# Kernel optimization log

Measured on AMD Instinct MI355X. Metric: run time of the kernel, lower is better.

The kernel has to match this reference:

```python
import jax, jax.numpy as jnp
import numpy as np

HEADS = 16
DIM_HEAD = 64
MAX_FREQ = 256.0  # lucidrains RotaryEmbedding(freqs_for='pixel', max_freq=256)


def axial_freqs(H, W, dim_head):
    # per-axis rotary dim = dim_head // 2 (RotaryEmbedding(dim=head_dim//2))
    d = dim_head // 2
    base = jnp.linspace(1.0, MAX_FREQ / 2.0, d // 2) * jnp.pi  # (d/2,)

    def axis(n):
        pos = jnp.linspace(-1.0, 1.0, n)              # pixel positions
        f = pos[:, None] * base                        # (n, d/2)
        return jnp.repeat(f, 2, axis=-1)               # (n, d) interleaved pairs

    fh = jnp.broadcast_to(axis(H)[:, None, :], (H, W, d))
    fw = jnp.broadcast_to(axis(W)[None, :, :], (H, W, d))
    return jnp.concatenate([fh, fw], axis=-1)          # (H, W, dim_head)


def apply_rope(t, freqs):
    # t: (B,T,H,W,h,d); freqs: (H,W,d)
    f = freqs[:, :, None, :]                           # broadcast over heads
    x = t.reshape(t.shape[:-1] + (t.shape[-1] // 2, 2))
    x1, x2 = x[..., 0], x[..., 1]
    rot = jnp.stack([-x2, x1], axis=-1).reshape(t.shape)  # rotate_half (interleaved)
    return t * jnp.cos(f) + rot * jnp.sin(f)


def setup_inputs() -> dict:
    key = jax.random.key(0)
    k1, k2, k3 = jax.random.split(key, 3)
    B, T, H, W, D = 1, 8, 32, 32, 1024
    inner = HEADS * DIM_HEAD
    x = jax.random.normal(k1, (B, T, H, W, D), dtype=jnp.float32)
    Wqkv = jax.random.normal(k2, (D, 3 * inner), dtype=jnp.float32) * 0.02
    Wout = jax.random.normal(k3, (inner, D), dtype=jnp.float32) * 0.02
    bout = jnp.zeros((D,), dtype=jnp.float32)
    return {"x": x, "Wqkv": Wqkv, "Wout": Wout, "bout": bout}


def reference(x, Wqkv, Wout, bout):
    B, T, H, W, D = x.shape
    qkv = x @ Wqkv                                     # (B,T,H,W,3*inner)
    q, k, v = jnp.split(qkv, 3, axis=-1)
    shp = (B, T, H, W, HEADS, DIM_HEAD)
    q, k, v = q.reshape(shp), k.reshape(shp), v.reshape(shp)
    freqs = axial_freqs(H, W, DIM_HEAD)
    q = apply_rope(q, freqs)
    k = apply_rope(k, freqs)
    S = H * W
    q = q.reshape(B * T, S, HEADS, DIM_HEAD)
    k = k.reshape(B * T, S, HEADS, DIM_HEAD)
    v = v.reshape(B * T, S, HEADS, DIM_HEAD)
    scale = 1.0 / np.sqrt(DIM_HEAD).astype(np.float32)
    att = jnp.einsum('bshd,bthd->bhst', q, k) * scale  # (BT, h, S, S)
    att = jax.nn.softmax(att, axis=-1)
    o = jnp.einsum('bhst,bthd->bshd', att, v)          # (BT, S, h, d)
    o = o.reshape(B, T, H, W, HEADS * DIM_HEAD)
    return o @ Wout + bout
```

## Files before the change

kernel.cpp:

```cpp
#include <hip/hip_runtime.h>
#include <math.h>

#define DMODEL 1024
#define NQKV   3072
#define SEQ    1024
#define NH     16
#define DH     64
#define HS     (SEQ*DH)
constexpr float PI_F   = 3.14159265358979323846f;
constexpr float LOG2E  = 1.44269504088896f;

typedef _Float16 half8   __attribute__((ext_vector_type(8)));
typedef _Float16 half4   __attribute__((ext_vector_type(4)));
typedef float    floatx4 __attribute__((ext_vector_type(4)));

__device__ __forceinline__ void gload_lds16(const _Float16* g, _Float16* l) {
    __builtin_amdgcn_global_load_lds(
        (const __attribute__((address_space(1))) unsigned int*)g,
        (__attribute__((address_space(3)))       unsigned int*)l,
        16, 0, 0);
}

__global__ __launch_bounds__(256) void cvt_f16(
    const float* __restrict__ in, _Float16* __restrict__ out, int n)
{
    int i = (blockIdx.x*256 + threadIdx.x)*8;
    if (i >= n) return;
    float4 a = *(const float4*)(in + i);
    float4 b = *(const float4*)(in + i + 4);
    half8 h;
    h[0]=(_Float16)a.x; h[1]=(_Float16)a.y; h[2]=(_Float16)a.z; h[3]=(_Float16)a.w;
    h[4]=(_Float16)b.x; h[5]=(_Float16)b.y; h[6]=(_Float16)b.z; h[7]=(_Float16)b.w;
    *(half8*)(out + i) = h;
}

__global__ __launch_bounds__(256) void tr_cvt(
    const float* __restrict__ in, _Float16* __restrict__ out, int R, int C)
{
    __shared__ float T[32][33];
    const int bx = blockIdx.x, by = blockIdx.y;
    const int tx = threadIdx.x & 31, ty = threadIdx.x >> 5;
#pragma unroll
    for (int i = 0; i < 4; ++i)
        T[ty + i*8][tx] = in[(size_t)(by*32 + ty + i*8)*C + bx*32 + tx];
    __syncthreads();
#pragma unroll
    for (int i = 0; i < 4; ++i)
        out[(size_t)(bx*32 + ty + i*8)*R + by*32 + tx] = (_Float16)T[tx][ty + i*8];
}

#define G1_BM 256
#define G1_BN 256
#define G1_BK 64

__global__ __launch_bounds__(512) void gemm1_f16(
    const _Float16* __restrict__ A, const _Float16* __restrict__ Bt,
    _Float16* __restrict__ C, int M, int N, int K)
{
    __shared__ _Float16 As[2][G1_BM*G1_BK] __attribute__((aligned(16)));
    __shared__ _Float16 Bs[2][G1_BN*G1_BK] __attribute__((aligned(16)));

    const int tid  = threadIdx.x;
    const int w    = tid >> 6, lane = tid & 63, quad = lane >> 4, l = lane & 15;
    const int wm   = (w >> 2)*128, wn = (w & 3)*64;

    int bid = blockIdx.y*gridDim.x + blockIdx.x;
    const int per = (gridDim.x*gridDim.y) >> 3;
    bid = (bid & 7)*per + (bid >> 3);
    const int bx = bid % gridDim.x, by = bid / gridDim.x;
    const int m0 = by*G1_BM, n0 = bx*G1_BN;

    const int sr  = tid >> 3;
    const int scg = (tid & 7) ^ (sr & 7);
    const _Float16* ga = A  + (size_t)(m0 + sr)*K + scg*8;
    const _Float16* gb = Bt + (size_t)(n0 + sr)*K + scg*8;

#define G1_STAGE_A(buf, kt, s) \
    gload_lds16(ga + (size_t)(s)*64*K + (size_t)(kt)*G1_BK, \
                &As[buf][(s)*4096 + w*512])
#define G1_STAGE_B(buf, kt, s) \
    gload_lds16(gb + (size_t)(s)*64*K + (size_t)(kt)*G1_BK, \
                &Bs[buf][(s)*4096 + w*512])
#define G1_RD_A(buf, mt, kh) \
    (*(half8*)&As[buf][(wm + (mt)*16 + l)*64 + ((((kh)*4 + quad) ^ (l & 7))*8)])
#define G1_RD_B(buf, nt, kh) \
    (*(half8*)&Bs[buf][(wn + (nt)*16 + l)*64 + ((((kh)*4 + quad) ^ (l & 7))*8)])

    floatx4 acc[8][4];
#pragma unroll
    for (int i = 0; i < 8; ++i)
#pragma unroll
        for (int j = 0; j < 4; ++j)
#pragma unroll
            for (int r = 0; r < 4; ++r) acc[i][j][r] = 0.f;

#pragma unroll
    for (int s = 0; s < 4; ++s) G1_STAGE_A(0, 0, s);
#pragma unroll
    for (int s = 0; s < 4; ++s) G1_STAGE_B(0, 0, s);
    asm volatile("s_waitcnt vmcnt(0)" ::: "memory");
    __builtin_amdgcn_s_barrier();
    __builtin_amdgcn_sched_barrier(0);

    const int KT = K / G1_BK;
    for (int kt = 0; kt < KT; ++kt) {
        const int cur = kt & 1, nxt = cur ^ 1;
        const bool pf = (kt + 1 < KT);
        half8 a0[4], a1[4], b0[2], b1[2];

#pragma unroll
        for (int mt = 0; mt < 4; ++mt) { a0[mt] = G1_RD_A(cur, mt, 0); a1[mt] = G1_RD_A(cur, mt, 1); }
#pragma unroll
        for (int nt = 0; nt < 2; ++nt) { b0[nt] = G1_RD_B(cur, nt, 0); b1[nt] = G1_RD_B(cur, nt, 1); }
        if (pf) { G1_STAGE_A(nxt, kt+1, 0); G1_STAGE_A(nxt, kt+1, 1);
                  G1_STAGE_B(nxt, kt+1, 0); G1_STAGE_B(nxt, kt+1, 1); }
        __builtin_amdgcn_s_barrier();
        asm volatile("s_waitcnt lgkmcnt(0)" ::: "memory");
        __builtin_amdgcn_sched_barrier(0);
        __builtin_amdgcn_s_setprio(1);
#pragma unroll
        for (int mt = 0; mt < 4; ++mt)
#pragma unroll
            for (int nt = 0; nt < 2; ++nt) {
                acc[mt][nt] = __builtin_amdgcn_mfma_f32_16x16x32_f16(a0[mt], b0[nt], acc[mt][nt], 0, 0, 0);
                acc[mt][nt] = __builtin_amdgcn_mfma_f32_16x16x32_f16(a1[mt], b1[nt], acc[mt][nt], 0, 0, 0);
            }
        __builtin_amdgcn_s_setprio(0);
        __builtin_amdgcn_s_barrier();

#pragma unroll
        for (int nt = 0; nt < 2; ++nt) { b0[nt] = G1_RD_B(cur, nt+2, 0); b1[nt] = G1_RD_B(cur, nt+2, 1); }
        if (pf) { G1_STAGE_A(nxt, kt+1, 2); G1_STAGE_A(nxt, kt+1, 3);
                  G1_STAGE_B(nxt, kt+1, 2); G1_STAGE_B(nxt, kt+1, 3); }
        __builtin_amdgcn_s_barrier();
        asm volatile("s_waitcnt lgkmcnt(0)" ::: "memory");
        __builtin_amdgcn_sched_barrier(0);
        __builtin_amdgcn_s_setprio(1);
#pragma unroll
        for (int mt = 0; mt < 4; ++mt)
#pragma unroll
            for (int nt = 0; nt < 2; ++nt) {
                acc[mt][nt+2] = __builtin_amdgcn_mfma_f32_16x16x32_f16(a0[mt], b0[nt], acc[mt][nt+2], 0, 0, 0);
                acc[mt][nt+2] = __builtin_amdgcn_mfma_f32_16x16x32_f16(a1[mt], b1[nt], acc[mt][nt+2], 0, 0, 0);
            }
        __builtin_amdgcn_s_setprio(0);
        __builtin_amdgcn_s_barrier();

#pragma unroll
        for (int mt = 0; mt < 4; ++mt) { a0[mt] = G1_RD_A(cur, mt+4, 0); a1[mt] = G1_RD_A(cur, mt+4, 1); }
        __builtin_amdgcn_s_barrier();
        asm volatile("s_waitcnt lgkmcnt(0)" ::: "memory");
        __builtin_amdgcn_sched_barrier(0);
        __builtin_amdgcn_s_setprio(1);
#pragma unroll
        for (int mt = 0; mt < 4; ++mt)
#pragma unroll
            for (int nt = 0; nt < 2; ++nt) {
                acc[mt+4][nt+2] = __builtin_amdgcn_mfma_f32_16x16x32_f16(a0[mt], b0[nt], acc[mt+4][nt+2], 0, 0, 0);
                acc[mt+4][nt+2] = __builtin_amdgcn_mfma_f32_16x16x32_f16(a1[mt], b1[nt], acc[mt+4][nt+2], 0, 0, 0);
            }
        __builtin_amdgcn_s_setprio(0);
        __builtin_amdgcn_s_barrier();

#pragma unroll
        for (int nt = 0; nt < 2; ++nt) { b0[nt] = G1_RD_B(cur, nt, 0); b1[nt] = G1_RD_B(cur, nt, 1); }
        __builtin_amdgcn_s_barrier();
        asm volatile("s_waitcnt lgkmcnt(0)" ::: "memory");
        __builtin_amdgcn_sched_barrier(0);
        __builtin_amdgcn_s_setprio(1);
#pragma unroll
        for (int mt = 0; mt < 4; ++mt)
#pragma unroll
            for (int nt = 0; nt < 2; ++nt) {
                acc[mt+4][nt] = __builtin_amdgcn_mfma_f32_16x16x32_f16(a0[mt], b0[nt], acc[mt+4][nt], 0, 0, 0);
                acc[mt+4][nt] = __builtin_amdgcn_mfma_f32_16x16x32_f16(a1[mt], b1[nt], acc[mt+4][nt], 0, 0, 0);
            }
        __builtin_amdgcn_s_setprio(0);
        asm volatile("s_waitcnt vmcnt(0)" ::: "memory");
        __builtin_amdgcn_s_barrier();
        __builtin_amdgcn_sched_barrier(0);
    }

#pragma unroll
    for (int mt = 0; mt < 8; ++mt)
#pragma unroll
        for (int r = 0; r < 4; ++r) {
            size_t row = m0 + wm + mt*16 + quad*4 + r;
#pragma unroll
            for (int nt = 0; nt < 4; ++nt)
                C[row*N + n0 + wn + nt*16 + l] = (_Float16)acc[mt][nt][r];
        }
#undef G1_STAGE_A
#undef G1_STAGE_B
#undef G1_RD_A
#undef G1_RD_B
}

__global__ __launch_bounds__(256) void gemm2_f16(
    const _Float16* __restrict__ A, const _Float16* __restrict__ Bt,
    const float* __restrict__ bias, float* __restrict__ C, int M, int N, int K)
{
    __shared__ _Float16 As[128*32];
    __shared__ _Float16 Bs[128*32];
    const int tid = threadIdx.x;
    const int w = tid >> 6, lane = tid & 63, quad = lane >> 4, l = lane & 15;
    const int wm = (w & 1)*64, wn = (w >> 1)*64;
    const int m0 = blockIdx.y*128, n0 = blockIdx.x*128;

    const _Float16* a0 = A  + (size_t)(m0 + w*32      + (lane>>2))*K + (lane&3)*8;
    const _Float16* a1 = A  + (size_t)(m0 + w*32 + 16 + (lane>>2))*K + (lane&3)*8;
    const _Float16* b0 = Bt + (size_t)(n0 + w*32      + (lane>>2))*K + (lane&3)*8;
    const _Float16* b1 = Bt + (size_t)(n0 + w*32 + 16 + (lane>>2))*K + (lane&3)*8;
    _Float16* lA0 = As + w*1024;
    _Float16* lA1 = As + w*1024 + 512;
    _Float16* lB0 = Bs + w*1024;
    _Float16* lB1 = Bs + w*1024 + 512;

    floatx4 acc[4][4];
#pragma unroll
    for (int i = 0; i < 4; ++i)
#pragma unroll
        for (int j = 0; j < 4; ++j)
#pragma unroll
            for (int r = 0; r < 4; ++r) acc[i][j][r] = 0.f;

    for (int k0 = 0; k0 < K; k0 += 32) {
        __syncthreads();
        gload_lds16(a0, lA0); gload_lds16(a1, lA1);
        gload_lds16(b0, lB0); gload_lds16(b1, lB1);
        a0 += 32; a1 += 32; b0 += 32; b1 += 32;
        __syncthreads();
        half8 bf[4];
#pragma unroll
        for (int nt = 0; nt < 4; ++nt)
            bf[nt] = *(half8*)&Bs[(wn + nt*16 + l)*32 + quad*8];
#pragma unroll
        for (int mt = 0; mt < 4; ++mt) {
            half8 af = *(half8*)&As[(wm + mt*16 + l)*32 + quad*8];
#pragma unroll
            for (int nt = 0; nt < 4; ++nt)
                acc[mt][nt] = __builtin_amdgcn_mfma_f32_16x16x32_f16(af, bf[nt], acc[mt][nt], 0, 0, 0);
        }
    }
#pragma unroll
    for (int mt = 0; mt < 4; ++mt)
#pragma unroll
        for (int r = 0; r < 4; ++r) {
            size_t row = m0 + wm + mt*16 + quad*4 + r;
#pragma unroll
            for (int nt = 0; nt < 4; ++nt) {
                int col = n0 + wn + nt*16 + l;
                C[row*N + col] = acc[mt][nt][r] + bias[col];
            }
        }
}

__global__ __launch_bounds__(256) void rope_scatter(
    const _Float16* __restrict__ qkv,
    _Float16* __restrict__ qw, _Float16* __restrict__ kw,
    _Float16* __restrict__ vt)
{
    const int sc = blockIdx.x;
    const int bh = blockIdx.y;
    const int bt = bh >> 4, head = bh & 15;
    const int s0 = sc*64;
    const int tid = threadIdx.x;
    const int d0 = (tid & 7)*8;

    __shared__ _Float16 T[64][80];

#pragma unroll
    for (int half = 0; half < 2; ++half) {
        const int r = (tid >> 3) + half*32;
        const int s = s0 + r;
        const _Float16* src = qkv + (size_t)(bt*SEQ + s)*NQKV + head*DH + d0;
        half8 hq = *(const half8*)(src);
        half8 hk = *(const half8*)(src + DMODEL);
        half8 hv = *(const half8*)(src + 2*DMODEL);
        float fq[8], fk[8];
#pragma unroll
        for (int j = 0; j < 8; ++j) { fq[j] = (float)hq[j]; fk[j] = (float)hk[j]; }
        const int hp = s >> 5, wp = s & 31;
        const float ph = -1.0f + hp*(2.0f/31.0f);
        const float pw = -1.0f + wp*(2.0f/31.0f);
#pragma unroll
        for (int p = 0; p < 4; ++p) {
            int pg = (d0 >> 1) + p;
            float pos = (pg < 16) ? ph : pw;
            int   gi  = (pg < 16) ? pg : (pg - 16);
            float th  = pos * ((1.0f + gi*(127.0f/15.0f)) * PI_F);
            float sn, cs;
            sincosf(th, &sn, &cs);
            float q1 = fq[2*p], q2 = fq[2*p+1];
            fq[2*p]   = q1*cs - q2*sn;
            fq[2*p+1] = q2*cs + q1*sn;
            float k1 = fk[2*p], k2 = fk[2*p+1];
            fk[2*p]   = k1*cs - k2*sn;
            fk[2*p+1] = k2*cs + k1*sn;
        }
        half8 oq, ok;
        const float qsc = 0.125f * LOG2E;
#pragma unroll
        for (int j = 0; j < 8; ++j) {
            oq[j] = (_Float16)(fq[j]*qsc);
            ok[j] = (_Float16)fk[j];
        }
        *(half8*)(qw + (size_t)bh*HS + (size_t)s*DH + d0) = oq;
        *(half8*)(kw + (size_t)bh*HS + (size_t)s*DH + d0) = ok;
#pragma unroll
        for (int j = 0; j < 8; ++j) T[d0 + j][r] = hv[j];
    }
    __syncthreads();
    const int d = tid >> 2, so = (tid & 3)*16;
    half8 v0 = *(half8*)&T[d][so];
    half8 v1 = *(half8*)&T[d][so + 8];
    _Float16* dst = vt + (size_t)bh*HS + (size_t)d*SEQ + s0 + so;
    *(half8*)dst       = v0;
    *(half8*)(dst + 8) = v1;
}

#define BC  64
#define LDH 68

__global__ __launch_bounds__(256) void attn_mfma(
    const _Float16* __restrict__ qw, const _Float16* __restrict__ kw,
    const _Float16* __restrict__ vt, _Float16* __restrict__ om)
{
    const int qc = blockIdx.x;
    const int bh = blockIdx.y;
    const int tid  = threadIdx.x;
    const int w    = tid >> 6;
    const int lane = tid & 63;
    const int quad = lane >> 4;
    const int l    = lane & 15;

    __shared__ _Float16 Ks[2][BC][LDH];
    __shared__ _Float16 Vs[2][DH][LDH];
    __shared__ _Float16 Ps[4][32][LDH];
    __shared__ float    Ls[4][32];

    const _Float16* qp = qw + (size_t)bh*HS + (size_t)(qc*128 + w*32)*DH;
    const _Float16* kp = kw + (size_t)bh*HS;
    const _Float16* vp = vt + (size_t)bh*HS;

    half8 qf[2][2];
#pragma unroll
    for (int qt = 0; qt < 2; ++qt) {
        qf[qt][0] = *(const half8*)(qp + (size_t)(qt*16 + l)*DH + quad*8);
        qf[qt][1] = *(const half8*)(qp + (size_t)(qt*16 + l)*DH + quad*8 + 32);
    }

    const int rs = tid >> 3;
    const int cs = (tid & 7)*8;

    half8 kr0 = *(const half8*)(kp + (size_t)rs*DH + cs);
    half8 kr1 = *(const half8*)(kp + (size_t)(rs+32)*DH + cs);
    half8 vr0 = *(const half8*)(vp + (size_t)rs*SEQ + cs);
    half8 vr1 = *(const half8*)(vp + (size_t)(rs+32)*SEQ + cs);
    *(half8*)&Ks[0][rs][cs]    = kr0;
    *(half8*)&Ks[0][rs+32][cs] = kr1;
    *(half8*)&Vs[0][rs][cs]    = vr0;
    *(half8*)&Vs[0][rs+32][cs] = vr1;

    floatx4 Of[2][4];
#pragma unroll
    for (int qt = 0; qt < 2; ++qt)
#pragma unroll
        for (int dt = 0; dt < 4; ++dt)
#pragma unroll
            for (int r = 0; r < 4; ++r) Of[qt][dt][r] = 0.f;
    float lsum[2] = {0.f, 0.f};

    __syncthreads();

    for (int kc = 0; kc < SEQ/BC; ++kc) {
        const int cur = kc & 1;
        if (kc < SEQ/BC - 1) {
            const _Float16* kn = kp + (size_t)(kc+1)*BC*DH;
            const _Float16* vn = vp + (size_t)(kc+1)*BC;
            kr0 = *(const half8*)(kn + (size_t)rs*DH + cs);
            kr1 = *(const half8*)(kn + (size_t)(rs+32)*DH + cs);
            vr0 = *(const half8*)(vn + (size_t)rs*SEQ + cs);
            vr1 = *(const half8*)(vn + (size_t)(rs+32)*SEQ + cs);
        }

        floatx4 Sf[2][4];
#pragma unroll
        for (int kg = 0; kg < 4; ++kg) {
            half8 af0 = *(half8*)&Ks[cur][kg*16 + l][quad*8];
            half8 af1 = *(half8*)&Ks[cur][kg*16 + l][quad*8 + 32];
#pragma unroll
            for (int qt = 0; qt < 2; ++qt) {
                floatx4 a;
#pragma unroll
                for (int r = 0; r < 4; ++r) a[r] = 0.f;
                a = __builtin_amdgcn_mfma_f32_16x16x32_f16(af0, qf[qt][0], a, 0, 0, 0);
                a = __builtin_amdgcn_mfma_f32_16x16x32_f16(af1, qf[qt][1], a, 0, 0, 0);
                Sf[qt][kg] = a;
            }
        }
#pragma unroll
        for (int qt = 0; qt < 2; ++qt)
#pragma unroll
            for (int kg = 0; kg < 4; ++kg) {
                half4 p4;
#pragma unroll
                for (int r = 0; r < 4; ++r) {
                    float p = __builtin_amdgcn_exp2f(Sf[qt][kg][r]);
                    lsum[qt] += p;
                    p4[r] = (_Float16)p;
                }
                *(half4*)&Ps[w][qt*16 + l][kg*16 + quad*4] = p4;
            }
        half8 pa[2][2];
#pragma unroll
        for (int qt = 0; qt < 2; ++qt) {
            pa[qt][0] = *(half8*)&Ps[w][qt*16 + l][quad*8];
            pa[qt][1] = *(half8*)&Ps[w][qt*16 + l][quad*8 + 32];
        }
#pragma unroll
        for (int dt = 0; dt < 4; ++dt) {
            half8 vb0 = *(half8*)&Vs[cur][dt*16 + l][quad*8];
            half8 vb1 = *(half8*)&Vs[cur][dt*16 + l][quad*8 + 32];
#pragma unroll
            for (int qt = 0; qt < 2; ++qt) {
                Of[qt][dt] = __builtin_amdgcn_mfma_f32_16x16x32_f16(pa[qt][0], vb0, Of[qt][dt], 0, 0, 0);
                Of[qt][dt] = __builtin_amdgcn_mfma_f32_16x16x32_f16(pa[qt][1], vb1, Of[qt][dt], 0, 0, 0);
            }
        }

        if (kc < SEQ/BC - 1) {
            *(half8*)&Ks[1-cur][rs][cs]    = kr0;
            *(half8*)&Ks[1-cur][rs+32][cs] = kr1;
            *(half8*)&Vs[1-cur][rs][cs]    = vr0;
            *(half8*)&Vs[1-cur][rs+32][cs] = vr1;
        }
        __syncthreads();
    }

#pragma unroll
    for (int qt = 0; qt < 2; ++qt) {
        lsum[qt] += __shfl_xor(lsum[qt], 16);
        lsum[qt] += __shfl_xor(lsum[qt], 32);
        if (quad == 0) Ls[w][qt*16 + l] = lsum[qt];
    }
    const int bt = bh >> 4, head = bh & 15;
    _Float16* opf = om + (size_t)(bt*SEQ + qc*128 + w*32)*DMODEL + head*DH;
#pragma unroll
    for (int qt = 0; qt < 2; ++qt) {
        float inv[4];
#pragma unroll
        for (int r = 0; r < 4; ++r) inv[r] = 1.0f / Ls[w][qt*16 + quad*4 + r];
#pragma unroll
        for (int dt = 0; dt < 4; ++dt)
#pragma unroll
            for (int r = 0; r < 4; ++r)
                opf[(size_t)(qt*16 + quad*4 + r)*DMODEL + dt*16 + l] =
                    (_Float16)(Of[qt][dt][r]*inv[r]);
    }
}

extern "C" void kernel_launch(void* const* d_in, const int* in_sizes, int n_in,
                              void* d_out, int out_size, void* d_ws, size_t ws_size,
                              hipStream_t stream)
{
    const float* x    = (const float*)d_in[0];
    const float* Wqkv = (const float*)d_in[1];
    const float* Wout = (const float*)d_in[2];
    const float* bout = (const float*)d_in[3];
    float* out = (float*)d_out;

    _Float16* ws   = (_Float16*)d_ws;
    _Float16* Xh   = ws;
    _Float16* Wqkt = ws + 8388608;
    _Float16* Wot  = ws + 11534336;
    _Float16* qkvt = ws + 12582912;
    _Float16* qw   = ws + 37748736;
    _Float16* kw   = ws + 46137344;
    _Float16* vt   = ws + 54525952;
    _Float16* om   = qkvt;

    hipLaunchKernelGGL(cvt_f16, dim3(4096), dim3(256), 0, stream,
                       x, Xh, 8388608);
    hipLaunchKernelGGL(tr_cvt, dim3(96, 32), dim3(256), 0, stream,
                       Wqkv, Wqkt, 1024, 3072);
    hipLaunchKernelGGL(tr_cvt, dim3(32, 32), dim3(256), 0, stream,
                       Wout, Wot, 1024, 1024);
    hipLaunchKernelGGL(gemm1_f16, dim3(12, 32), dim3(512), 0, stream,
                       Xh, Wqkt, qkvt, 8192, NQKV, DMODEL);
    hipLaunchKernelGGL(rope_scatter, dim3(16, 128), dim3(256), 0, stream,
                       qkvt, qw, kw, vt);
    hipLaunchKernelGGL(attn_mfma, dim3(8, 128), dim3(256), 0, stream,
                       qw, kw, vt, om);
    hipLaunchKernelGGL(gemm2_f16, dim3(8, 64), dim3(256), 0, stream,
                       om, Wot, bout, out, 8192, DMODEL, DMODEL);
}
```

Before: 271.4 us.

## Split gemm1 K-tile into two half stages with finer-grained vmcnt pipelining

Restructures the QKV GEMM's shared-memory tiles into two 32-wide K halves, each with its own swizzle, and issues global-to-LDS loads per half. Waits use partial vmcnt/lgkmcnt counts instead of full drains, and the number of barriers per K-step is reduced so loads overlap with MFMA work. The goal is to hide global load latency and cut synchronisation stalls. It relies on hand-counted waitcnt values, which are fragile if the compiler reorders or adds memory ops.

```diff
diff --git a/kernel.cpp b/kernel.cpp
--- a/kernel.cpp
+++ b/kernel.cpp
@@ -49,16 +49,12 @@
         out[(size_t)(bx*32 + ty + i*8)*R + by*32 + tx] = (_Float16)T[tx][ty + i*8];
 }
 
-#define G1_BM 256
-#define G1_BN 256
-#define G1_BK 64
-
 __global__ __launch_bounds__(512) void gemm1_f16(
     const _Float16* __restrict__ A, const _Float16* __restrict__ Bt,
     _Float16* __restrict__ C, int M, int N, int K)
 {
-    __shared__ _Float16 As[2][G1_BM*G1_BK] __attribute__((aligned(16)));
-    __shared__ _Float16 Bs[2][G1_BN*G1_BK] __attribute__((aligned(16)));
+    __shared__ _Float16 As[2][2][8192] __attribute__((aligned(16)));
+    __shared__ _Float16 Bs[2][2][8192] __attribute__((aligned(16)));
 
     const int tid  = threadIdx.x;
     const int w    = tid >> 6, lane = tid & 63, quad = lane >> 4, l = lane & 15;
@@ -68,23 +64,24 @@
     const int per = (gridDim.x*gridDim.y) >> 3;
     bid = (bid & 7)*per + (bid >> 3);
     const int bx = bid % gridDim.x, by = bid / gridDim.x;
-    const int m0 = by*G1_BM, n0 = bx*G1_BN;
-
-    const int sr  = tid >> 3;
-    const int scg = (tid & 7) ^ (sr & 7);
-    const _Float16* ga = A  + (size_t)(m0 + sr)*K + scg*8;
-    const _Float16* gb = Bt + (size_t)(n0 + sr)*K + scg*8;
-
-#define G1_STAGE_A(buf, kt, s) \
-    gload_lds16(ga + (size_t)(s)*64*K + (size_t)(kt)*G1_BK, \
-                &As[buf][(s)*4096 + w*512])
-#define G1_STAGE_B(buf, kt, s) \
-    gload_lds16(gb + (size_t)(s)*64*K + (size_t)(kt)*G1_BK, \
-                &Bs[buf][(s)*4096 + w*512])
-#define G1_RD_A(buf, mt, kh) \
-    (*(half8*)&As[buf][(wm + (mt)*16 + l)*64 + ((((kh)*4 + quad) ^ (l & 7))*8)])
-#define G1_RD_B(buf, nt, kh) \
-    (*(half8*)&Bs[buf][(wn + (nt)*16 + l)*64 + ((((kh)*4 + quad) ^ (l & 7))*8)])
+    const int m0 = by*256, n0 = bx*256;
+
+    const int rs   = tid >> 2;
+    const int csrc = (tid & 3) ^ ((tid >> 3) & 3);
+    const _Float16* ga = A  + (size_t)(m0 + rs)*K + csrc*8;
+    const _Float16* gb = Bt + (size_t)(n0 + rs)*K + csrc*8;
+    const int swz8 = (quad ^ ((l >> 1) & 3))*8;
+
+#define G1_STAGE_A(buf, kt, h) do { \
+    gload_lds16(ga + (size_t)(kt)*64 + (h)*32,                 &As[buf][h][w*512]); \
+    gload_lds16(ga + (size_t)(kt)*64 + (h)*32 + (size_t)128*K, &As[buf][h][4096 + w*512]); \
+} while (0)
+#define G1_STAGE_B(buf, kt, h) do { \
+    gload_lds16(gb + (size_t)(kt)*64 + (h)*32,                 &Bs[buf][h][w*512]); \
+    gload_lds16(gb + (size_t)(kt)*64 + (h)*32 + (size_t)128*K, &Bs[buf][h][4096 + w*512]); \
+} while (0)
+#define G1_RD_A(buf, h, mt) (*(half8*)&As[buf][h][(wm + (mt)*16 + l)*32 + swz8])
+#define G1_RD_B(buf, h, nt) (*(half8*)&Bs[buf][h][(wn + (nt)*16 + l)*32 + swz8])
 
     floatx4 acc[8][4];
 #pragma unroll
@@ -94,91 +91,80 @@
 #pragma unroll
             for (int r = 0; r < 4; ++r) acc[i][j][r] = 0.f;
 
-#pragma unroll
-    for (int s = 0; s < 4; ++s) G1_STAGE_A(0, 0, s);
-#pragma unroll
-    for (int s = 0; s < 4; ++s) G1_STAGE_B(0, 0, s);
-    asm volatile("s_waitcnt vmcnt(0)" ::: "memory");
-    __builtin_amdgcn_s_barrier();
-    __builtin_amdgcn_sched_barrier(0);
-
-    const int KT = K / G1_BK;
+    G1_STAGE_A(0, 0, 0);
+    G1_STAGE_B(0, 0, 0);
+    G1_STAGE_A(0, 0, 1);
+    G1_STAGE_B(0, 0, 1);
+
+    const int KT = K / 64;
     for (int kt = 0; kt < KT; ++kt) {
         const int cur = kt & 1, nxt = cur ^ 1;
         const bool pf = (kt + 1 < KT);
-        half8 a0[4], a1[4], b0[2], b1[2];
-
-#pragma unroll
-        for (int mt = 0; mt < 4; ++mt) { a0[mt] = G1_RD_A(cur, mt, 0); a1[mt] = G1_RD_A(cur, mt, 1); }
-#pragma unroll
-        for (int nt = 0; nt < 2; ++nt) { b0[nt] = G1_RD_B(cur, nt, 0); b1[nt] = G1_RD_B(cur, nt, 1); }
-        if (pf) { G1_STAGE_A(nxt, kt+1, 0); G1_STAGE_A(nxt, kt+1, 1);
-                  G1_STAGE_B(nxt, kt+1, 0); G1_STAGE_B(nxt, kt+1, 1); }
+        half8 af[8], bf[4];
+
+        if (pf) G1_STAGE_A(nxt, kt+1, 0);
+        if (pf) asm volatile("s_waitcnt vmcnt(6)" ::: "memory");
+        else    asm volatile("s_waitcnt vmcnt(4)" ::: "memory");
         __builtin_amdgcn_s_barrier();
+        __builtin_amdgcn_sched_barrier(0);
+#pragma unroll
+        for (int mt = 0; mt < 4; ++mt) af[mt] = G1_RD_A(cur, 0, mt);
+#pragma unroll
+        for (int nt = 0; nt < 4; ++nt) bf[nt] = G1_RD_B(cur, 0, nt);
+        __builtin_amdgcn_sched_barrier(0);
+#pragma unroll
+        for (int mt = 4; mt < 8; ++mt) af[mt] = G1_RD_A(cur, 0, mt);
+        if (pf) G1_STAGE_B(nxt, kt+1, 0);
+        asm volatile("s_waitcnt lgkmcnt(4)" ::: "memory");
+        __builtin_amdgcn_sched_barrier(0);
+        __builtin_amdgcn_s_setprio(1);
+#pragma unroll
+        for (int mt = 0; mt < 4; ++mt)
+#pragma unroll
+            for (int nt = 0; nt < 4; ++nt)
+                acc[mt][nt] = __builtin_amdgcn_mfma_f32_16x16x32_f16(af[mt], bf[nt], acc[mt][nt], 0, 0, 0);
+        __builtin_amdgcn_s_setprio(0);
         asm volatile("s_waitcnt lgkmcnt(0)" ::: "memory");
         __builtin_amdgcn_sched_barrier(0);
         __builtin_amdgcn_s_setprio(1);
 #pragma unroll
+        for (int mt = 4; mt < 8; ++mt)
+#pragma unroll
+            for (int nt = 0; nt < 4; ++nt)
+                acc[mt][nt] = __builtin_amdgcn_mfma_f32_16x16x32_f16(af[mt], bf[nt], acc[mt][nt], 0, 0, 0);
+        __builtin_amdgcn_s_setprio(0);
+
+        if (pf) G1_STAGE_A(nxt, kt+1, 1);
+        if (pf) asm volatile("s_waitcnt vmcnt(6)" ::: "memory");
+        else    asm volatile("s_waitcnt vmcnt(0)" ::: "memory");
+        __builtin_amdgcn_s_barrier();
+        __builtin_amdgcn_sched_barrier(0);
+#pragma unroll
+        for (int mt = 0; mt < 4; ++mt) af[mt] = G1_RD_A(cur, 1, mt);
+#pragma unroll
+        for (int nt = 0; nt < 4; ++nt) bf[nt] = G1_RD_B(cur, 1, nt);
+        __builtin_amdgcn_sched_barrier(0);
+#pragma unroll
+        for (int mt = 4; mt < 8; ++mt) af[mt] = G1_RD_A(cur, 1, mt);
+        if (pf) G1_STAGE_B(nxt, kt+1, 1);
+        asm volatile("s_waitcnt lgkmcnt(4)" ::: "memory");
+        __builtin_amdgcn_sched_barrier(0);
+        __builtin_amdgcn_s_setprio(1);
+#pragma unroll
         for (int mt = 0; mt < 4; ++mt)
 #pragma unroll
-            for (int nt = 0; nt < 2; ++nt) {
-                acc[mt][nt] = __builtin_amdgcn_mfma_f32_16x16x32_f16(a0[mt], b0[nt], acc[mt][nt], 0, 0, 0);
-                acc[mt][nt] = __builtin_amdgcn_mfma_f32_16x16x32_f16(a1[mt], b1[nt], acc[mt][nt], 0, 0, 0);
-            }
+            for (int nt = 0; nt < 4; ++nt)
+                acc[mt][nt] = __builtin_amdgcn_mfma_f32_16x16x32_f16(af[mt], bf[nt], acc[mt][nt], 0, 0, 0);
         __builtin_amdgcn_s_setprio(0);
-        __builtin_amdgcn_s_barrier();
-
-#pragma unroll
-        for (int nt = 0; nt < 2; ++nt) { b0[nt] = G1_RD_B(cur, nt+2, 0); b1[nt] = G1_RD_B(cur, nt+2, 1); }
-        if (pf) { G1_STAGE_A(nxt, kt+1, 2); G1_STAGE_A(nxt, kt+1, 3);
-                  G1_STAGE_B(nxt, kt+1, 2); G1_STAGE_B(nxt, kt+1, 3); }
-        __builtin_amdgcn_s_barrier();
         asm volatile("s_waitcnt lgkmcnt(0)" ::: "memory");
         __builtin_amdgcn_sched_barrier(0);
         __builtin_amdgcn_s_setprio(1);
 #pragma unroll
-        for (int mt = 0; mt < 4; ++mt)
-#pragma unroll
-            for (int nt = 0; nt < 2; ++nt) {
-                acc[mt][nt+2] = __builtin_amdgcn_mfma_f32_16x16x32_f16(a0[mt], b0[nt], acc[mt][nt+2], 0, 0, 0);
-                acc[mt][nt+2] = __builtin_amdgcn_mfma_f32_16x16x32_f16(a1[mt], b1[nt], acc[mt][nt+2], 0, 0, 0);
-            }
+        for (int mt = 4; mt < 8; ++mt)
+#pragma unroll
+            for (int nt = 0; nt < 4; ++nt)
+                acc[mt][nt] = __builtin_amdgcn_mfma_f32_16x16x32_f16(af[mt], bf[nt], acc[mt][nt], 0, 0, 0);
         __builtin_amdgcn_s_setprio(0);
-        __builtin_amdgcn_s_barrier();
-
-#pragma unroll
-        for (int mt = 0; mt < 4; ++mt) { a0[mt] = G1_RD_A(cur, mt+4, 0); a1[mt] = G1_RD_A(cur, mt+4, 1); }
-        __builtin_amdgcn_s_barrier();
-        asm volatile("s_waitcnt lgkmcnt(0)" ::: "memory");
-        __builtin_amdgcn_sched_barrier(0);
-        __builtin_amdgcn_s_setprio(1);
-#pragma unroll
-        for (int mt = 0; mt < 4; ++mt)
-#pragma unroll
-            for (int nt = 0; nt < 2; ++nt) {
-                acc[mt+4][nt+2] = __builtin_amdgcn_mfma_f32_16x16x32_f16(a0[mt], b0[nt], acc[mt+4][nt+2], 0, 0, 0);
-                acc[mt+4][nt+2] = __builtin_amdgcn_mfma_f32_16x16x32_f16(a1[mt], b1[nt], acc[mt+4][nt+2], 0, 0, 0);
-            }
-        __builtin_amdgcn_s_setprio(0);
-        __builtin_amdgcn_s_barrier();
-
-#pragma unroll
-        for (int nt = 0; nt < 2; ++nt) { b0[nt] = G1_RD_B(cur, nt, 0); b1[nt] = G1_RD_B(cur, nt, 1); }
-        __builtin_amdgcn_s_barrier();
-        asm volatile("s_waitcnt lgkmcnt(0)" ::: "memory");
-        __builtin_amdgcn_sched_barrier(0);
-        __builtin_amdgcn_s_setprio(1);
-#pragma unroll
-        for (int mt = 0; mt < 4; ++mt)
-#pragma unroll
-            for (int nt = 0; nt < 2; ++nt) {
-                acc[mt+4][nt] = __builtin_amdgcn_mfma_f32_16x16x32_f16(a0[mt], b0[nt], acc[mt+4][nt], 0, 0, 0);
-                acc[mt+4][nt] = __builtin_amdgcn_mfma_f32_16x16x32_f16(a1[mt], b1[nt], acc[mt+4][nt], 0, 0, 0);
-            }
-        __builtin_amdgcn_s_setprio(0);
-        asm volatile("s_waitcnt vmcnt(0)" ::: "memory");
-        __builtin_amdgcn_s_barrier();
-        __builtin_amdgcn_sched_barrier(0);
     }
 
 #pragma unroll
```

Result: faster. 261.1 us (-3.8%).
